# Kernel optimization log

Measured on AMD Instinct MI355X. Metric: run time of the kernel, lower is better.

## Reference

```python
import jax, jax.numpy as jnp
import numpy as np

BN_EPS = 1e-5

def conv1x1(x, w, b):
    # x: [B,C,H,W], w: [O,C], b: [O]
    return jnp.einsum('bchw,oc->bohw', x, w) + b[None, :, None, None]

def maxpool2x2(x):
    B, C, H, W = x.shape
    return x.reshape(B, C, H // 2, 2, W // 2, 2).max(axis=(3, 5))

def setup_inputs() -> dict:
    key = jax.random.key(0)
    ks = jax.random.split(key, 11)
    B, C, H, W = 8, 256, 64, 64
    Ci = C // 2  # inter_channels = 128
    s_in = 1.0 / np.sqrt(C)
    s_int = 1.0 / np.sqrt(Ci)
    return {
        'x': jax.random.normal(ks[0], (B, C, H, W), jnp.float32),
        'theta_w': jax.random.uniform(ks[1], (Ci, C), jnp.float32, -s_in, s_in),
        'theta_b': jax.random.uniform(ks[2], (Ci,), jnp.float32, -s_in, s_in),
        'phi_w': jax.random.uniform(ks[3], (Ci, C), jnp.float32, -s_in, s_in),
        'phi_b': jax.random.uniform(ks[4], (Ci,), jnp.float32, -s_in, s_in),
        'g_w': jax.random.uniform(ks[5], (Ci, C), jnp.float32, -s_in, s_in),
        'g_b': jax.random.uniform(ks[6], (Ci,), jnp.float32, -s_in, s_in),
        'W_w': jax.random.uniform(ks[7], (C, Ci), jnp.float32, -s_int, s_int),
        'W_b': jax.random.uniform(ks[8], (C,), jnp.float32, -s_int, s_int),
        'bn_gamma': jax.random.normal(ks[9], (C,), jnp.float32) * 0.1 + 1.0,
        'bn_beta': jax.random.normal(ks[10], (C,), jnp.float32) * 0.1,
    }

def reference(x, theta_w, theta_b, phi_w, phi_b, g_w, g_b, W_w, W_b, bn_gamma, bn_beta):
    B, C, H, W = x.shape
    Ci = theta_w.shape[0]
    # g and phi are sub-sampled (2x2 maxpool) after the 1x1 conv
    g_x = maxpool2x2(conv1x1(x, g_w, g_b)).reshape(B, Ci, -1)        # [B,Ci,M]
    g_x = g_x.transpose(0, 2, 1)                                     # [B,M,Ci]
    theta_x = conv1x1(x, theta_w, theta_b).reshape(B, Ci, -1)        # [B,Ci,N]
    theta_x = theta_x.transpose(0, 2, 1)                             # [B,N,Ci]
    phi_x = maxpool2x2(conv1x1(x, phi_w, phi_b)).reshape(B, Ci, -1)  # [B,Ci,M]
    f = jnp.einsum('bnc,bcm->bnm', theta_x, phi_x)                   # [B,N,M]
    f_div_C = jax.nn.softmax(f, axis=-1)
    y = jnp.einsum('bnm,bmc->bnc', f_div_C, g_x)                     # [B,N,Ci]
    y = y.transpose(0, 2, 1).reshape(B, Ci, H, W)
    # 1x1 conv + BatchNorm2d (training-mode batch statistics)
    W_y = conv1x1(y, W_w, W_b)
    mean = W_y.mean(axis=(0, 2, 3))
    var = W_y.var(axis=(0, 2, 3))
    W_y = (W_y - mean[None, :, None, None]) * jax.lax.rsqrt(var + BN_EPS)[None, :, None, None]
    W_y = W_y * bn_gamma[None, :, None, None] + bn_beta[None, :, None, None]
    return W_y + x
```

## Files before the change

### kernel.cpp

```cpp
#include <hip/hip_runtime.h>
#include <hip/hip_bf16.h>
#include <cstdint>
#include <math.h>

using bf16 = __hip_bfloat16;
typedef __attribute__((ext_vector_type(8))) short bf16x8;
typedef __attribute__((ext_vector_type(4))) float f32x4;

#define DEV __device__ __forceinline__

DEV float b2f(unsigned short u) { return __uint_as_float(((uint32_t)u) << 16); }
DEV float bfl(bf16 h) { return __bfloat162float(h); }
DEV short f2bs(float f) { bf16 h = __float2bfloat16(f); return *(short*)&h; }
DEV uint32_t pk2(float a, float b) {
  return (uint32_t)(unsigned short)f2bs(a) |
         ((uint32_t)(unsigned short)f2bs(b) << 16);
}
DEV float ldv(const void* p, int isbf, int i) {
  return isbf ? bfl(((const bf16*)p)[i]) : ((const float*)p)[i];
}

DEV bf16x8 load_wfrag(const void* w, int isbf, int row, int K, int off) {
  bf16x8 r;
  if (isbf) {
    r = *(const bf16x8*)((const short*)w + (size_t)row * K + off);
  } else {
    const float* f = (const float*)w + (size_t)row * K + off;
    float4 a = *(const float4*)f, b = *(const float4*)(f + 4);
    r[0] = f2bs(a.x); r[1] = f2bs(a.y); r[2] = f2bs(a.z); r[3] = f2bs(a.w);
    r[4] = f2bs(b.x); r[5] = f2bs(b.y); r[6] = f2bs(b.z); r[7] = f2bs(b.w);
  }
  return r;
}

__global__ __launch_bounds__(256) void sniff_kernel(
    const unsigned short* __restrict__ xr, int* __restrict__ flag)
{
  int tid = threadIdx.x;
  int good = 0;
  for (int k = tid; k < 16384; k += 256) {
    unsigned short u = xr[2 * k];
    int e = (u >> 7) & 0xFF;
    good += (e >= 0x6A && e <= 0x86) ? 1 : 0;
  }
  __shared__ int r[256];
  r[tid] = good;
  __syncthreads();
  for (int off = 128; off; off >>= 1) {
    if (tid < off) r[tid] += r[tid + off];
    __syncthreads();
  }
  if (tid == 0) *flag = (r[0] > 9830) ? 1 : 0;
}

__global__ __launch_bounds__(256) void transpose_x(
    const void* __restrict__ x, short* __restrict__ xT, const int* __restrict__ flag)
{
  const int isbf = *flag;
  __shared__ short lt[64 * 71];
  const int n0 = blockIdx.x * 64, c0 = blockIdx.y * 64, b = blockIdx.z;
  const int tid = threadIdx.x;
  for (int it = 0; it < 4; ++it) {
    int idx4 = it * 256 + tid;
    int ci = idx4 >> 4, n4 = (idx4 & 15) * 4;
    size_t go = ((size_t)(b * 256 + c0 + ci)) * 4096 + n0 + n4;
    if (isbf) {
      ushort4 v = *(const ushort4*)((const unsigned short*)x + go);
      lt[ci * 71 + n4 + 0] = v.x; lt[ci * 71 + n4 + 1] = v.y;
      lt[ci * 71 + n4 + 2] = v.z; lt[ci * 71 + n4 + 3] = v.w;
    } else {
      float4 v = *(const float4*)((const float*)x + go);
      lt[ci * 71 + n4 + 0] = f2bs(v.x); lt[ci * 71 + n4 + 1] = f2bs(v.y);
      lt[ci * 71 + n4 + 2] = f2bs(v.z); lt[ci * 71 + n4 + 3] = f2bs(v.w);
    }
  }
  __syncthreads();
  for (int it = 0; it < 4; ++it) {
    int idx4 = it * 256 + tid;
    int n = idx4 >> 4, c4 = (idx4 & 15) * 4;
    ushort4 v;
    v.x = (unsigned short)lt[(c4 + 0) * 71 + n];
    v.y = (unsigned short)lt[(c4 + 1) * 71 + n];
    v.z = (unsigned short)lt[(c4 + 2) * 71 + n];
    v.w = (unsigned short)lt[(c4 + 3) * 71 + n];
    *(ushort4*)(xT + ((size_t)(b * 4096 + n0 + n)) * 256 + c0 + c4) = v;
  }
}

__global__ __launch_bounds__(256) void conv_t_k(
    const short* __restrict__ xT, const void* __restrict__ w,
    const void* __restrict__ bias, short* __restrict__ out,
    const int* __restrict__ flag)
{
  const int isbf = *flag;
  __shared__ short sh[64 * 264];
  const int b = blockIdx.y, nbase = blockIdx.x * 64, tid = threadIdx.x;
  const int ln = tid & 15, q = (tid >> 4) & 3, wv = tid >> 6;
  for (int it = 0; it < 16; ++it) {
    int idx4 = it * 256 + tid;
    int n = idx4 >> 6, c4 = (idx4 & 63) * 4;
    *(ushort4*)&sh[n * 264 + c4] =
        *(const ushort4*)(xT + ((size_t)(b * 4096 + nbase + n)) * 256 + c4);
  }
  __syncthreads();
  f32x4 zero = {0.f, 0.f, 0.f, 0.f};
  f32x4 acc[4][2];
  for (int nt = 0; nt < 4; ++nt) for (int ti = 0; ti < 2; ++ti) acc[nt][ti] = zero;

  for (int kk = 0; kk < 8; ++kk) {
    int off = kk * 32 + q * 8;
    bf16x8 a[4];
    #pragma unroll
    for (int nt = 0; nt < 4; ++nt)
      a[nt] = *(const bf16x8*)&sh[(16 * nt + ln) * 264 + off];
    #pragma unroll
    for (int ti = 0; ti < 2; ++ti) {
      bf16x8 bw = load_wfrag(w, isbf, 16 * (2 * wv + ti) + ln, 256, off);
      #pragma unroll
      for (int nt = 0; nt < 4; ++nt)
        acc[nt][ti] = __builtin_amdgcn_mfma_f32_16x16x32_bf16(a[nt], bw, acc[nt][ti], 0, 0, 0);
    }
  }
  __syncthreads();
  float bv[2];
  for (int ti = 0; ti < 2; ++ti) bv[ti] = ldv(bias, isbf, 16 * (2 * wv + ti) + ln);
  for (int nt = 0; nt < 4; ++nt)
    for (int ti = 0; ti < 2; ++ti)
      for (int r = 0; r < 4; ++r)
        sh[(16 * nt + q * 4 + r) * 136 + 16 * (2 * wv + ti) + ln] =
            f2bs(acc[nt][ti][r] + bv[ti]);
  __syncthreads();
  for (int it = 0; it < 8; ++it) {
    int idx4 = it * 256 + tid;
    int n = idx4 >> 5, c4 = (idx4 & 31) * 4;
    *(ushort4*)(out + ((size_t)(b * 4096 + nbase + n)) * 128 + c4) =
        *(const ushort4*)&sh[n * 136 + c4];
  }
}

template<int CO, int K>
__global__ __launch_bounds__(256) void conv_n_k(
    const short* __restrict__ inp, const void* __restrict__ w,
    const void* __restrict__ bias, short* __restrict__ out,
    const int* __restrict__ flag)
{
  const int isbf = *flag;
  constexpr int XS = 64 * (K + 8);
  constexpr int OS = CO * 68;
  __shared__ short sh[(XS > OS ? XS : OS)];
  const int b = blockIdx.y, nbase = blockIdx.x * 64, tid = threadIdx.x;
  const int ln = tid & 15, q = (tid >> 4) & 3, wv = tid >> 6;
  constexpr int TPW = CO / 64;
  constexpr int KS = (K == 256) ? 6 : 5;
  for (int it = 0; it < 64 * K / 1024; ++it) {
    int idx4 = it * 256 + tid;
    int n = idx4 >> KS, c4 = (idx4 & ((K / 4) - 1)) * 4;
    *(ushort4*)&sh[n * (K + 8) + c4] =
        *(const ushort4*)(inp + ((size_t)(b * 4096 + nbase + n)) * K + c4);
  }
  __syncthreads();
  f32x4 zero = {0.f, 0.f, 0.f, 0.f};
  f32x4 acc[TPW][4];
  for (int ti = 0; ti < TPW; ++ti) for (int nt = 0; nt < 4; ++nt) acc[ti][nt] = zero;

  for (int kk = 0; kk < K / 32; ++kk) {
    int off = kk * 32 + q * 8;
    bf16x8 bx[4];
    #pragma unroll
    for (int nt = 0; nt < 4; ++nt)
      bx[nt] = *(const bf16x8*)&sh[(16 * nt + ln) * (K + 8) + off];
    #pragma unroll
    for (int ti = 0; ti < TPW; ++ti) {
      bf16x8 aw = load_wfrag(w, isbf, 16 * (TPW * wv + ti) + ln, K, off);
      #pragma unroll
      for (int nt = 0; nt < 4; ++nt)
        acc[ti][nt] = __builtin_amdgcn_mfma_f32_16x16x32_bf16(aw, bx[nt], acc[ti][nt], 0, 0, 0);
    }
  }
  __syncthreads();
  for (int ti = 0; ti < TPW; ++ti)
    for (int r = 0; r < 4; ++r) {
      int co = 16 * (TPW * wv + ti) + q * 4 + r;
      float bb = ldv(bias, isbf, co);
      for (int nt = 0; nt < 4; ++nt)
        sh[co * 68 + 16 * nt + ln] = f2bs(acc[ti][nt][r] + bb);
    }
  __syncthreads();
  for (int it = 0; it < 64 * CO / 1024; ++it) {
    int idx4 = it * 256 + tid;
    int co = idx4 >> 4, n4 = (idx4 & 15) * 4;
    *(ushort4*)(out + ((size_t)(b * CO + co)) * 4096 + nbase + n4) =
        *(const ushort4*)&sh[co * 68 + n4];
  }
}

__global__ __launch_bounds__(256) void pool_phi_kernel(
    const short* __restrict__ pc, short* __restrict__ phi)
{
  int idx = blockIdx.x * 256 + threadIdx.x;
  int ci = idx & 127, m = (idx >> 7) & 1023, b = idx >> 17;
  int mh = m >> 5, mw = m & 31;
  const short* p = pc + ((size_t)(b * 4096 + (mh * 2) * 64 + mw * 2)) * 128 + ci;
  float v = fmaxf(fmaxf(b2f(p[0]), b2f(p[128])),
                  fmaxf(b2f(p[64 * 128]), b2f(p[65 * 128])));
  phi[idx] = f2bs(v);
}

__global__ __launch_bounds__(256) void pool_g_kernel(
    const short* __restrict__ gc, short* __restrict__ g)
{
  int idx = blockIdx.x * 256 + threadIdx.x;
  int m = idx & 1023, bc = idx >> 10;
  int mh = m >> 5, mw = m & 31;
  const short* p = gc + (size_t)bc * 4096 + mh * 128 + mw * 2;
  float v = fmaxf(fmaxf(b2f(p[0]), b2f(p[1])), fmaxf(b2f(p[64]), b2f(p[65])));
  g[idx] = f2bs(v);
}

__global__ __launch_bounds__(256) void attn_kernel(
    const short* __restrict__ theta, const short* __restrict__ phi,
    const short* __restrict__ g, short* __restrict__ y)
{
  __shared__ short th[64 * 136];
  __shared__ short ph[64 * 136];
  __shared__ short gl[128 * 72];
  __shared__ short Pl[64 * 72];
  const int b = blockIdx.y, nbase = blockIdx.x * 64, tid = threadIdx.x;
  const int ln = tid & 15, q = (tid >> 4) & 3, wv = tid >> 6;

  for (int it = 0; it < 8; ++it) {
    int idx4 = it * 256 + tid;
    int n = idx4 >> 5, c4 = (idx4 & 31) * 4;
    *(ushort4*)&th[n * 136 + c4] =
        *(const ushort4*)(theta + ((size_t)(b * 4096 + nbase + n)) * 128 + c4);
  }

  f32x4 zero = {0.f, 0.f, 0.f, 0.f};
  f32x4 yacc[8], lacc = zero;
  for (int t = 0; t < 8; ++t) yacc[t] = zero;
  bf16x8 ones;
  #pragma unroll
  for (int j = 0; j < 8; ++j) ones[j] = 0x3F80;

  for (int mc = 0; mc < 16; ++mc) {
    __syncthreads();
    for (int it = 0; it < 8; ++it) {
      int idx4 = it * 256 + tid;
      int m = idx4 >> 5, c4 = (idx4 & 31) * 4;
      *(ushort4*)&ph[m * 136 + c4] =
          *(const ushort4*)(phi + ((size_t)(b * 1024 + mc * 64 + m)) * 128 + c4);
    }
    for (int it = 0; it < 8; ++it) {
      int idx4 = it * 256 + tid;
      int ci = idx4 >> 4, m4 = (idx4 & 15) * 4;
      *(ushort4*)&gl[ci * 72 + m4] =
          *(const ushort4*)(g + ((size_t)(b * 128 + ci)) * 1024 + mc * 64 + m4);
    }
    __syncthreads();

    bf16x8 a[4];
    #pragma unroll
    for (int kk = 0; kk < 4; ++kk)
      a[kk] = *(const bf16x8*)&th[(16 * wv + ln) * 136 + kk * 32 + q * 8];
    #pragma unroll
    for (int t = 0; t < 4; ++t) {
      f32x4 s = zero;
      #pragma unroll
      for (int kk = 0; kk < 4; ++kk) {
        bf16x8 bp = *(const bf16x8*)&ph[(16 * t + ln) * 136 + kk * 32 + q * 8];
        s = __builtin_amdgcn_mfma_f32_16x16x32_bf16(a[kk], bp, s, 0, 0, 0);
      }
      #pragma unroll
      for (int r = 0; r < 4; ++r)
        Pl[(16 * wv + q * 4 + r) * 72 + 16 * t + ln] =
            f2bs(__expf(fminf(s[r], 80.f)));
    }
    bf16x8 ap[2];
    #pragma unroll
    for (int kk = 0; kk < 2; ++kk)
      ap[kk] = *(const bf16x8*)&Pl[(16 * wv + ln) * 72 + kk * 32 + q * 8];
    #pragma unroll
    for (int kk = 0; kk < 2; ++kk)
      lacc = __builtin_amdgcn_mfma_f32_16x16x32_bf16(ap[kk], ones, lacc, 0, 0, 0);
    #pragma unroll
    for (int t = 0; t < 8; ++t) {
      #pragma unroll
      for (int kk = 0; kk < 2; ++kk) {
        bf16x8 bg = *(const bf16x8*)&gl[(16 * t + ln) * 72 + kk * 32 + q * 8];
        yacc[t] = __builtin_amdgcn_mfma_f32_16x16x32_bf16(ap[kk], bg, yacc[t], 0, 0, 0);
      }
    }
  }
  __syncthreads();

  float li[4];
  #pragma unroll
  for (int r = 0; r < 4; ++r) li[r] = 1.0f / lacc[r];
  for (int t = 0; t < 8; ++t)
    for (int r = 0; r < 4; ++r)
      ph[(16 * wv + q * 4 + r) * 136 + 16 * t + ln] = f2bs(yacc[t][r] * li[r]);
  __syncthreads();
  for (int it = 0; it < 8; ++it) {
    int idx4 = it * 256 + tid;
    int n = idx4 >> 5, c4 = (idx4 & 31) * 4;
    *(ushort4*)(y + ((size_t)(b * 4096 + nbase + n)) * 128 + c4) =
        *(const ushort4*)&ph[n * 136 + c4];
  }
}

__global__ __launch_bounds__(256, 4) void convW_k(
    const short* __restrict__ yb, const void* __restrict__ w,
    const void* __restrict__ bias, short* __restrict__ Wy,
    float* __restrict__ stats, const int* __restrict__ flag)
{
  const int isbf = *flag;
  __shared__ short sh[256 * 72];
  const int b = blockIdx.y, nbase = blockIdx.x * 64, tid = threadIdx.x;
  const int ln = tid & 15, q = (tid >> 4) & 3, wv = tid >> 6;

  for (int it = 0; it < 4; ++it) {
    int idx8 = it * 256 + tid;
    int n = idx8 >> 4, c8 = (idx8 & 15) * 8;
    *(uint4*)&sh[n * 136 + c8] =
        *(const uint4*)(yb + ((size_t)(b * 4096 + nbase + n)) * 128 + c8);
  }
  __syncthreads();
  f32x4 zero = {0.f, 0.f, 0.f, 0.f};
  f32x4 acc[4][4];
  for (int ti = 0; ti < 4; ++ti)
    for (int nt = 0; nt < 4; ++nt) acc[ti][nt] = zero;

  for (int kk = 0; kk < 4; ++kk) {
    int off = kk * 32 + q * 8;
    bf16x8 bx[4];
    #pragma unroll
    for (int nt = 0; nt < 4; ++nt)
      bx[nt] = *(const bf16x8*)&sh[(16 * nt + ln) * 136 + off];
    #pragma unroll
    for (int ti = 0; ti < 4; ++ti) {
      bf16x8 aw = load_wfrag(w, isbf, 16 * (4 * wv + ti) + ln, 128, off);
      #pragma unroll
      for (int nt = 0; nt < 4; ++nt)
        acc[ti][nt] = __builtin_amdgcn_mfma_f32_16x16x32_bf16(aw, bx[nt], acc[ti][nt], 0, 0, 0);
    }
  }
  __syncthreads();
  #pragma unroll
  for (int ti = 0; ti < 4; ++ti)
    #pragma unroll
    for (int r = 0; r < 4; ++r) {
      int co = 16 * (4 * wv + ti) + 4 * q + r;
      float bb = ldv(bias, isbf, co);
      #pragma unroll
      for (int nt = 0; nt < 4; ++nt)
        sh[co * 72 + 16 * nt + ln] = f2bs(acc[ti][nt][r] + bb);
    }
  __syncthreads();
  {
    int co = tid;
    float s = 0.f, s2 = 0.f;
    for (int i = 0; i < 64; ++i) {
      float v = b2f((unsigned short)sh[co * 72 + i]);
      s += v; s2 += v * v;
    }
    atomicAdd(&stats[co], s);
    atomicAdd(&stats[256 + co], s2);
  }
  for (int it = 0; it < 8; ++it) {
    int idx8 = it * 256 + tid;
    int co = idx8 >> 3, n8 = (idx8 & 7) * 8;
    *(uint4*)(Wy + ((size_t)(b * 256 + co)) * 4096 + nbase + n8) =
        *(const uint4*)&sh[co * 72 + n8];
  }
}

__global__ __launch_bounds__(256) void bn_apply4(
    const short* __restrict__ Wy, const void* __restrict__ x,
    const float* __restrict__ stats, const void* __restrict__ gamma,
    const void* __restrict__ beta, void* __restrict__ out,
    const int* __restrict__ flag)
{
  const int isbf = *flag;
  int t = blockIdx.x * 256 + threadIdx.x;
  int idx4 = t * 4;
  int c = (idx4 >> 12) & 255;
  float s = stats[c], s2 = stats[256 + c];
  float mean = s * (1.0f / 32768.0f);
  float var = fmaxf(s2 * (1.0f / 32768.0f) - mean * mean, 0.f);
  float scale = rsqrtf(var + 1e-5f) * ldv(gamma, isbf, c);
  float shift = ldv(beta, isbf, c) - mean * scale;
  ushort4 wy = *(const ushort4*)(Wy + idx4);
  float xv[4];
  if (isbf) {
    ushort4 xu = *(const ushort4*)((const unsigned short*)x + idx4);
    xv[0] = b2f(xu.x); xv[1] = b2f(xu.y); xv[2] = b2f(xu.z); xv[3] = b2f(xu.w);
  } else {
    float4 xf = *(const float4*)((const float*)x + idx4);
    xv[0] = xf.x; xv[1] = xf.y; xv[2] = xf.z; xv[3] = xf.w;
  }
  float v0 = b2f(wy.x) * scale + shift + xv[0];
  float v1 = b2f(wy.y) * scale + shift + xv[1];
  float v2 = b2f(wy.z) * scale + shift + xv[2];
  float v3 = b2f(wy.w) * scale + shift + xv[3];
  if (isbf) {
    uint2 o; o.x = pk2(v0, v1); o.y = pk2(v2, v3);
    *(uint2*)((unsigned short*)out + idx4) = o;
  } else {
    float4 o = make_float4(v0, v1, v2, v3);
    *(float4*)((float*)out + idx4) = o;
  }
}

extern "C" void kernel_launch(void* const* d_in, const int* in_sizes, int n_in,
                              void* d_out, int out_size, void* d_ws, size_t ws_size,
                              hipStream_t stream) {
  const void* x       = d_in[0];
  const void* theta_w = d_in[1];
  const void* theta_b = d_in[2];
  const void* phi_w   = d_in[3];
  const void* phi_b   = d_in[4];
  const void* g_w     = d_in[5];
  const void* g_b     = d_in[6];
  const void* W_w     = d_in[7];
  const void* W_b     = d_in[8];
  const void* gamma   = d_in[9];
  const void* beta    = d_in[10];

  char* wsb = (char*)d_ws;
  short* xT      = (short*)(wsb + 0);
  short* ybuf    = (short*)(wsb + 0);
  short* theta   = (short*)(wsb + 16777216);
  short* W_y     = (short*)(wsb + 16777216);
  short* scratch = (short*)(wsb + 25165824);
  short* phi     = (short*)(wsb + 33554432);
  short* gg      = (short*)(wsb + 35651584);
  float* stats   = (float*)(wsb + 37748736);
  int*   flag    = (int*)  (wsb + 37750784);

  dim3 blk(256);
  dim3 cgrid(64, 8);
  dim3 tgrid(64, 4, 8);

  hipMemsetAsync(stats, 0, 2048, stream);
  sniff_kernel<<<1, blk, 0, stream>>>((const unsigned short*)x, flag);
  transpose_x<<<tgrid, blk, 0, stream>>>(x, xT, flag);
  conv_t_k<<<cgrid, blk, 0, stream>>>(xT, theta_w, theta_b, theta, flag);
  conv_t_k<<<cgrid, blk, 0, stream>>>(xT, phi_w, phi_b, scratch, flag);
  pool_phi_kernel<<<4096, blk, 0, stream>>>(scratch, phi);
  conv_n_k<128, 256><<<cgrid, blk, 0, stream>>>(xT, g_w, g_b, scratch, flag);
  pool_g_kernel<<<4096, blk, 0, stream>>>(scratch, gg);
  attn_kernel<<<cgrid, blk, 0, stream>>>(theta, phi, gg, ybuf);
  convW_k<<<cgrid, blk, 0, stream>>>(ybuf, W_w, W_b, W_y, stats, flag);
  bn_apply4<<<8192, blk, 0, stream>>>(W_y, x, stats, gamma, beta, d_out, flag);
}
```

Measured before the change: 241.0 us.

## Restructure attention kernel to keep theta in registers and compute transposed products

```diff
diff --git a/kernel.cpp b/kernel.cpp
--- a/kernel.cpp
+++ b/kernel.cpp
@@ -217,94 +217,115 @@
   g[idx] = f2bs(v);
 }
 
-__global__ __launch_bounds__(256) void attn_kernel(
+__global__ __launch_bounds__(256, 3) void attn_kernel(
     const short* __restrict__ theta, const short* __restrict__ phi,
     const short* __restrict__ g, short* __restrict__ y)
 {
   __shared__ short th[64 * 136];
   __shared__ short ph[64 * 136];
   __shared__ short gl[128 * 72];
-  __shared__ short Pl[64 * 72];
+  short* Pl = th;
   const int b = blockIdx.y, nbase = blockIdx.x * 64, tid = threadIdx.x;
   const int ln = tid & 15, q = (tid >> 4) & 3, wv = tid >> 6;
 
-  for (int it = 0; it < 8; ++it) {
-    int idx4 = it * 256 + tid;
-    int n = idx4 >> 5, c4 = (idx4 & 31) * 4;
-    *(ushort4*)&th[n * 136 + c4] =
-        *(const ushort4*)(theta + ((size_t)(b * 4096 + nbase + n)) * 128 + c4);
-  }
+  for (int it = 0; it < 4; ++it) {
+    int idx8 = it * 256 + tid;
+    int n = idx8 >> 4, c8 = (idx8 & 15) * 8;
+    *(uint4*)&th[n * 136 + c8] =
+        *(const uint4*)(theta + ((size_t)(b * 4096 + nbase + n)) * 128 + c8);
+  }
+  __syncthreads();
+  bf16x8 bth[4][4];
+  #pragma unroll
+  for (int t = 0; t < 4; ++t)
+    #pragma unroll
+    for (int kk = 0; kk < 4; ++kk)
+      bth[t][kk] = *(const bf16x8*)&th[(16 * t + ln) * 136 + kk * 32 + q * 8];
+
+  bf16x8 onesA;
+  #pragma unroll
+  for (int j = 0; j < 8; ++j) onesA[j] = 0x3F80;
 
   f32x4 zero = {0.f, 0.f, 0.f, 0.f};
-  f32x4 yacc[8], lacc = zero;
-  for (int t = 0; t < 8; ++t) yacc[t] = zero;
-  bf16x8 ones;
-  #pragma unroll
-  for (int j = 0; j < 8; ++j) ones[j] = 0x3F80;
+  f32x4 yacc[2][4], lacc[4];
+  for (int ti = 0; ti < 2; ++ti)
+    for (int t = 0; t < 4; ++t) yacc[ti][t] = zero;
+  for (int t = 0; t < 4; ++t) lacc[t] = zero;
+
+  const short* pp = phi + ((size_t)b * 1024) * 128;
+  const short* gp = g + ((size_t)b * 128) * 1024;
 
   for (int mc = 0; mc < 16; ++mc) {
     __syncthreads();
-    for (int it = 0; it < 8; ++it) {
-      int idx4 = it * 256 + tid;
-      int m = idx4 >> 5, c4 = (idx4 & 31) * 4;
-      *(ushort4*)&ph[m * 136 + c4] =
-          *(const ushort4*)(phi + ((size_t)(b * 1024 + mc * 64 + m)) * 128 + c4);
-    }
-    for (int it = 0; it < 8; ++it) {
-      int idx4 = it * 256 + tid;
-      int ci = idx4 >> 4, m4 = (idx4 & 15) * 4;
-      *(ushort4*)&gl[ci * 72 + m4] =
-          *(const ushort4*)(g + ((size_t)(b * 128 + ci)) * 1024 + mc * 64 + m4);
+    for (int it = 0; it < 4; ++it) {
+      int idx8 = it * 256 + tid;
+      int m = idx8 >> 4, c8 = (idx8 & 15) * 8;
+      *(uint4*)&ph[m * 136 + c8] =
+          *(const uint4*)(pp + ((size_t)(mc * 64 + m)) * 128 + c8);
+    }
+    for (int it = 0; it < 4; ++it) {
+      int idx8 = it * 256 + tid;
+      int ci = idx8 >> 3, m8 = (idx8 & 7) * 8;
+      *(uint4*)&gl[ci * 72 + m8] =
+          *(const uint4*)(gp + (size_t)ci * 1024 + mc * 64 + m8);
     }
     __syncthreads();
 
-    bf16x8 a[4];
+    bf16x8 ap[4];
     #pragma unroll
     for (int kk = 0; kk < 4; ++kk)
-      a[kk] = *(const bf16x8*)&th[(16 * wv + ln) * 136 + kk * 32 + q * 8];
+      ap[kk] = *(const bf16x8*)&ph[(16 * wv + ln) * 136 + kk * 32 + q * 8];
     #pragma unroll
     for (int t = 0; t < 4; ++t) {
       f32x4 s = zero;
       #pragma unroll
-      for (int kk = 0; kk < 4; ++kk) {
-        bf16x8 bp = *(const bf16x8*)&ph[(16 * t + ln) * 136 + kk * 32 + q * 8];
-        s = __builtin_amdgcn_mfma_f32_16x16x32_bf16(a[kk], bp, s, 0, 0, 0);
-      }
-      #pragma unroll
-      for (int r = 0; r < 4; ++r)
-        Pl[(16 * wv + q * 4 + r) * 72 + 16 * t + ln] =
-            f2bs(__expf(fminf(s[r], 80.f)));
-    }
-    bf16x8 ap[2];
-    #pragma unroll
-    for (int kk = 0; kk < 2; ++kk)
-      ap[kk] = *(const bf16x8*)&Pl[(16 * wv + ln) * 72 + kk * 32 + q * 8];
-    #pragma unroll
-    for (int kk = 0; kk < 2; ++kk)
-      lacc = __builtin_amdgcn_mfma_f32_16x16x32_bf16(ap[kk], ones, lacc, 0, 0, 0);
-    #pragma unroll
-    for (int t = 0; t < 8; ++t) {
-      #pragma unroll
-      for (int kk = 0; kk < 2; ++kk) {
-        bf16x8 bg = *(const bf16x8*)&gl[(16 * t + ln) * 72 + kk * 32 + q * 8];
-        yacc[t] = __builtin_amdgcn_mfma_f32_16x16x32_bf16(ap[kk], bg, yacc[t], 0, 0, 0);
-      }
-    }
-  }
-  __syncthreads();
+      for (int kk = 0; kk < 4; ++kk)
+        s = __builtin_amdgcn_mfma_f32_16x16x32_bf16(ap[kk], bth[t][kk], s, 0, 0, 0);
+      uint2 uu;
+      uu.x = pk2(__expf(fminf(s[0], 80.f)), __expf(fminf(s[1], 80.f)));
+      uu.y = pk2(__expf(fminf(s[2], 80.f)), __expf(fminf(s[3], 80.f)));
+      *(uint2*)&Pl[(16 * t + ln) * 72 + 16 * wv + 4 * q] = uu;
+    }
+    __syncthreads();
+
+    #pragma unroll
+    for (int kk = 0; kk < 2; ++kk) {
+      bf16x8 bp[4], ag[2];
+      #pragma unroll
+      for (int t = 0; t < 4; ++t)
+        bp[t] = *(const bf16x8*)&Pl[(16 * t + ln) * 72 + kk * 32 + q * 8];
+      #pragma unroll
+      for (int ti = 0; ti < 2; ++ti)
+        ag[ti] = *(const bf16x8*)&gl[(16 * (2 * wv + ti) + ln) * 72 + kk * 32 + q * 8];
+      #pragma unroll
+      for (int ti = 0; ti < 2; ++ti)
+        #pragma unroll
+        for (int t = 0; t < 4; ++t)
+          yacc[ti][t] = __builtin_amdgcn_mfma_f32_16x16x32_bf16(ag[ti], bp[t], yacc[ti][t], 0, 0, 0);
+      #pragma unroll
+      for (int t = 0; t < 4; ++t)
+        lacc[t] = __builtin_amdgcn_mfma_f32_16x16x32_bf16(onesA, bp[t], lacc[t], 0, 0, 0);
+    }
+  }
 
   float li[4];
   #pragma unroll
-  for (int r = 0; r < 4; ++r) li[r] = 1.0f / lacc[r];
-  for (int t = 0; t < 8; ++t)
-    for (int r = 0; r < 4; ++r)
-      ph[(16 * wv + q * 4 + r) * 136 + 16 * t + ln] = f2bs(yacc[t][r] * li[r]);
-  __syncthreads();
-  for (int it = 0; it < 8; ++it) {
-    int idx4 = it * 256 + tid;
-    int n = idx4 >> 5, c4 = (idx4 & 31) * 4;
-    *(ushort4*)(y + ((size_t)(b * 4096 + nbase + n)) * 128 + c4) =
-        *(const ushort4*)&ph[n * 136 + c4];
+  for (int t = 0; t < 4; ++t) li[t] = 1.0f / lacc[t][0];
+  #pragma unroll
+  for (int ti = 0; ti < 2; ++ti)
+    #pragma unroll
+    for (int t = 0; t < 4; ++t) {
+      uint2 uu;
+      uu.x = pk2(yacc[ti][t][0] * li[t], yacc[ti][t][1] * li[t]);
+      uu.y = pk2(yacc[ti][t][2] * li[t], yacc[ti][t][3] * li[t]);
+      *(uint2*)&ph[(16 * t + ln) * 136 + 32 * wv + 16 * ti + 4 * q] = uu;
+    }
+  __syncthreads();
+  for (int it = 0; it < 4; ++it) {
+    int idx8 = it * 256 + tid;
+    int n = idx8 >> 4, c8 = (idx8 & 15) * 8;
+    *(uint4*)(y + ((size_t)(b * 4096 + nbase + n)) * 128 + c8) =
+        *(const uint4*)&ph[n * 136 + c8];
   }
 }
 
```

After: 248.4 us. 3.1% more time.
